# Optimization experiments

Hardware: AMD Instinct MI355X
Metric: run time of the kernel (lower is better)

The kernel has to match this reference:

```python
import jax, jax.numpy as jnp
import numpy as np

EPS = 1e-12
SHRINK = 0.0025

def _l2norm(x, axis=1):
    return x / jnp.maximum(jnp.linalg.norm(x, axis=axis, keepdims=True), EPS)

def setup_inputs() -> dict:
    key = jax.random.key(0)
    ks = jax.random.split(key, 6)
    N, C, H, W = 32, 512, 32, 32
    mem_dim, spatial = 512, H * W
    hid = spatial // 2
    x = jax.random.normal(ks[0], (N, C, H, W), dtype=jnp.float32)
    memory = jax.random.normal(ks[1], (mem_dim, spatial), dtype=jnp.float32)
    memory = _l2norm(memory, axis=1)  # buffer is L2-normalized at init
    w1 = jax.random.normal(ks[2], (hid, spatial), dtype=jnp.float32) * 0.02
    b1 = jax.random.normal(ks[3], (hid,), dtype=jnp.float32) * 0.02
    w2 = jax.random.normal(ks[4], (spatial, hid), dtype=jnp.float32) * 0.02
    b2 = jax.random.normal(ks[5], (spatial,), dtype=jnp.float32) * 0.02
    return {"x": x, "memory": memory, "w1": w1, "b1": b1, "w2": w2, "b2": b2}

def reference(x, memory, w1, b1, w2, b2):
    N, C, H, W = x.shape
    mem_dim = memory.shape[0]
    input_flat = x.reshape(N * C, H * W)
    input_norm = _l2norm(input_flat, axis=1)
    # shared MLP over memory bank: Linear -> ReLU -> Linear -> ReLU
    h = jax.nn.relu(memory @ w1.T + b1)
    mem_proc = jax.nn.relu(h @ w2.T + b2)
    memory_norm = _l2norm(mem_proc, axis=1)
    # addressing: cosine sim -> softmax -> hard shrink -> L1 renorm
    att = jax.nn.softmax(input_norm @ memory_norm.T, axis=1)  # [N*C, M]
    att = jax.nn.relu(att - SHRINK)
    att = att / jnp.maximum(att.sum(axis=1, keepdims=True), EPS)  # p=1 norm (att >= 0)
    output = (att @ memory_norm).reshape(N, C, H, W)
    att_channel_avg = att.reshape(N, C, mem_dim).mean(axis=1)  # [N, M]
    att_spatial = jnp.broadcast_to(att_channel_avg[:, :, None, None], (N, mem_dim, H, W))
    return output, att_spatial, input_flat, memory_norm, att
```

## Files before the change

### kernel.cpp

```cpp
#include <hip/hip_runtime.h>

typedef float  f32x4  __attribute__((ext_vector_type(4)));
typedef __bf16 bf16x8 __attribute__((ext_vector_type(8)));
typedef __bf16 bf16x4 __attribute__((ext_vector_type(4)));

#define L2EPS   1e-12f
#define SHRINKC 0.0025f


__device__ __forceinline__ bf16x8 pack_bf16(f32x4 v0, f32x4 v1) {
  bf16x8 r;
  r[0] = (__bf16)v0[0]; r[1] = (__bf16)v0[1]; r[2] = (__bf16)v0[2]; r[3] = (__bf16)v0[3];
  r[4] = (__bf16)v1[0]; r[5] = (__bf16)v1[1]; r[6] = (__bf16)v1[2]; r[7] = (__bf16)v1[3];
  return r;
}

__device__ __forceinline__ bf16x8 load_cvt_bf16x8(const float* p) {
  const f32x4* q = (const f32x4*)p;
  return pack_bf16(q[0], q[1]);
}

__device__ __forceinline__ float dot4(f32x4 v) {
  return v[0]*v[0] + v[1]*v[1] + v[2]*v[2] + v[3]*v[3];
}

__global__ __launch_bounds__(64) void gemm1(
    const float* __restrict__ A, const float* __restrict__ B,
    const float* __restrict__ bias, float* __restrict__ C,
    float* __restrict__ attsum) {
  const int bid = blockIdx.y * gridDim.x + blockIdx.x;
  attsum[bid * 64 + threadIdx.x] = 0.f;

  const int K = 1024, N = 512;
  const int r0   = blockIdx.x * 32;
  const int n0   = blockIdx.y * 32;
  const int lane = threadIdx.x & 63;
  const int quad = lane >> 4;
  const int m    = lane & 15;

  f32x4 acc[2][2] = {};
  for (int k0 = 0; k0 < K; k0 += 32) {
    const int kk = k0 + quad * 8;
    bf16x8 a[2], b[2];
    #pragma unroll
    for (int rg = 0; rg < 2; ++rg)
      a[rg] = load_cvt_bf16x8(A + (size_t)(r0 + rg * 16 + m) * K + kk);
    #pragma unroll
    for (int cf = 0; cf < 2; ++cf)
      b[cf] = load_cvt_bf16x8(B + (size_t)(n0 + cf * 16 + m) * K + kk);
    #pragma unroll
    for (int rg = 0; rg < 2; ++rg)
      #pragma unroll
      for (int cf = 0; cf < 2; ++cf)
        acc[rg][cf] = __builtin_amdgcn_mfma_f32_16x16x32_bf16(a[rg], b[cf], acc[rg][cf], 0, 0, 0);
  }
  #pragma unroll
  for (int rg = 0; rg < 2; ++rg)
    #pragma unroll
    for (int cf = 0; cf < 2; ++cf) {
      const int n = n0 + cf * 16 + m;
      const float bv = bias[n];
      #pragma unroll
      for (int vi = 0; vi < 4; ++vi) {
        const int r = r0 + rg * 16 + quad * 4 + vi;
        C[(size_t)r * N + n] = fmaxf(acc[rg][cf][vi] + bv, 0.f);
      }
    }
}

__global__ __launch_bounds__(64) void gemm2(
    const float* __restrict__ A, const float* __restrict__ B,
    const float* __restrict__ bias, float* __restrict__ C) {
  const int K = 512, N = 1024;
  const int r0   = blockIdx.x * 32;
  const int n0   = blockIdx.y * 32;
  const int lane = threadIdx.x & 63;
  const int quad = lane >> 4;
  const int m    = lane & 15;

  f32x4 acc[2][2] = {};
  for (int k0 = 0; k0 < K; k0 += 32) {
    const int kk = k0 + quad * 8;
    bf16x8 a[2], b[2];
    #pragma unroll
    for (int rg = 0; rg < 2; ++rg)
      a[rg] = load_cvt_bf16x8(A + (size_t)(r0 + rg * 16 + m) * K + kk);
    #pragma unroll
    for (int cf = 0; cf < 2; ++cf)
      b[cf] = load_cvt_bf16x8(B + (size_t)(n0 + cf * 16 + m) * K + kk);
    #pragma unroll
    for (int rg = 0; rg < 2; ++rg)
      #pragma unroll
      for (int cf = 0; cf < 2; ++cf)
        acc[rg][cf] = __builtin_amdgcn_mfma_f32_16x16x32_bf16(a[rg], b[cf], acc[rg][cf], 0, 0, 0);
  }
  #pragma unroll
  for (int rg = 0; rg < 2; ++rg)
    #pragma unroll
    for (int cf = 0; cf < 2; ++cf) {
      const int n = n0 + cf * 16 + m;
      const float bv = bias[n];
      #pragma unroll
      for (int vi = 0; vi < 4; ++vi) {
        const int r = r0 + rg * 16 + quad * 4 + vi;
        C[(size_t)r * N + n] = fmaxf(acc[rg][cf][vi] + bv, 0.f);
      }
    }
}

__global__ __launch_bounds__(256) void norm_rows(
    const float* __restrict__ mp, float* __restrict__ mn_f32,
    __bf16* __restrict__ mn_bf16) {
  const int r = blockIdx.x;
  const int tid = threadIdx.x;
  const f32x4 v = *(const f32x4*)(mp + (size_t)r * 1024 + tid * 4);
  float ss = dot4(v);
  #pragma unroll
  for (int d = 1; d < 64; d <<= 1) ss += __shfl_xor(ss, d);
  __shared__ float wsum[4];
  __shared__ float invs;
  if ((tid & 63) == 0) wsum[tid >> 6] = ss;
  __syncthreads();
  if (tid == 0) {
    float t = wsum[0] + wsum[1] + wsum[2] + wsum[3];
    invs = 1.f / fmaxf(sqrtf(t), L2EPS);
  }
  __syncthreads();
  const float iv = invs;
  f32x4 o = v * iv;
  *(f32x4*)(mn_f32 + (size_t)r * 1024 + tid * 4) = o;
  bf16x4 ob;
  ob[0] = (__bf16)o[0]; ob[1] = (__bf16)o[1]; ob[2] = (__bf16)o[2]; ob[3] = (__bf16)o[3];
  *(bf16x4*)(mn_bf16 + (size_t)r * 1024 + tid * 4) = ob;
}

__global__ __launch_bounds__(256) void attend(
    const float* __restrict__ x, const __bf16* __restrict__ Mn,
    const float* __restrict__ Mnf, float* __restrict__ out_flat,
    float* __restrict__ out_out, float* __restrict__ out_att,
    float* __restrict__ attsum) {
  __shared__ float red[2][4][32];
  const int r0   = blockIdx.x * 32;
  const int tid  = threadIdx.x;
  const int wave = tid >> 6;
  const int lane = tid & 63;
  const int quad = lane >> 4;
  const int m    = lane & 15;
  const int n0w  = wave * 128;

  float ss0 = 0.f, ss1 = 0.f;
  f32x4 acc[8][2] = {};
  for (int k0 = 0; k0 < 1024; k0 += 32) {
    const int kk = k0 + quad * 8;
    bf16x8 b[2];
    f32x4 v0a, v0b, v1a, v1b;
    {
      const f32x4* q = (const f32x4*)(x + (size_t)(r0 + m) * 1024 + kk);
      v0a = q[0]; v0b = q[1];
      b[0] = pack_bf16(v0a, v0b);
      ss0 += dot4(v0a) + dot4(v0b);
    }
    {
      const f32x4* q = (const f32x4*)(x + (size_t)(r0 + 16 + m) * 1024 + kk);
      v1a = q[0]; v1b = q[1];
      b[1] = pack_bf16(v1a, v1b);
      ss1 += dot4(v1a) + dot4(v1b);
    }
    if (wave == 0) {
      float* d0 = out_flat + (size_t)(r0 + m) * 1024 + kk;
      float* d1 = out_flat + (size_t)(r0 + 16 + m) * 1024 + kk;
      *(f32x4*)d0 = v0a; *(f32x4*)(d0 + 4) = v0b;
      *(f32x4*)d1 = v1a; *(f32x4*)(d1 + 4) = v1b;
    }
    #pragma unroll
    for (int nf = 0; nf < 8; ++nf) {
      const bf16x8 a = *(const bf16x8*)(Mn + (size_t)(n0w + nf * 16 + m) * 1024 + kk);
      acc[nf][0] = __builtin_amdgcn_mfma_f32_16x16x32_bf16(a, b[0], acc[nf][0], 0, 0, 0);
      acc[nf][1] = __builtin_amdgcn_mfma_f32_16x16x32_bf16(a, b[1], acc[nf][1], 0, 0, 0);
    }
  }
  ss0 += __shfl_xor(ss0, 16); ss0 += __shfl_xor(ss0, 32);
  ss1 += __shfl_xor(ss1, 16); ss1 += __shfl_xor(ss1, 32);
  const float iv0 = 1.f / fmaxf(sqrtf(ss0), L2EPS);
  const float iv1 = 1.f / fmaxf(sqrtf(ss1), L2EPS);

  float se0 = 0.f, se1 = 0.f;
  #pragma unroll
  for (int nf = 0; nf < 8; ++nf)
    #pragma unroll
    for (int vi = 0; vi < 4; ++vi) {
      const float e0 = __expf(acc[nf][0][vi] * iv0);
      const float e1 = __expf(acc[nf][1][vi] * iv1);
      acc[nf][0][vi] = e0; acc[nf][1][vi] = e1;
      se0 += e0; se1 += e1;
    }
  se0 += __shfl_xor(se0, 16); se0 += __shfl_xor(se0, 32);
  se1 += __shfl_xor(se1, 16); se1 += __shfl_xor(se1, 32);
  if (quad == 0) { red[0][wave][m] = se0; red[0][wave][16 + m] = se1; }
  __syncthreads();
  const float te0 = red[0][0][m] + red[0][1][m] + red[0][2][m] + red[0][3][m];
  const float te1 = red[0][0][16 + m] + red[0][1][16 + m] + red[0][2][16 + m] + red[0][3][16 + m];
  const float ie0 = 1.f / te0;
  const float ie1 = 1.f / te1;

  float rs0 = 0.f, rs1 = 0.f;
  #pragma unroll
  for (int nf = 0; nf < 8; ++nf)
    #pragma unroll
    for (int vi = 0; vi < 4; ++vi) {
      const float s0 = fmaxf(acc[nf][0][vi] * ie0 - SHRINKC, 0.f);
      const float s1 = fmaxf(acc[nf][1][vi] * ie1 - SHRINKC, 0.f);
      acc[nf][0][vi] = s0; acc[nf][1][vi] = s1;
      rs0 += s0; rs1 += s1;
    }
  rs0 += __shfl_xor(rs0, 16); rs0 += __shfl_xor(rs0, 32);
  rs1 += __shfl_xor(rs1, 16); rs1 += __shfl_xor(rs1, 32);
  if (quad == 0) { red[1][wave][m] = rs0; red[1][wave][16 + m] = rs1; }
  __syncthreads();
  const float tr0 = red[1][0][m] + red[1][1][m] + red[1][2][m] + red[1][3][m];
  const float tr1 = red[1][0][16 + m] + red[1][1][16 + m] + red[1][2][16 + m] + red[1][3][16 + m];
  const float ir0 = 1.f / fmaxf(tr0, L2EPS);
  const float ir1 = 1.f / fmaxf(tr1, L2EPS);

  #pragma unroll
  for (int nf = 0; nf < 8; ++nf) {
    acc[nf][0] *= ir0;
    acc[nf][1] *= ir1;
    *(f32x4*)(out_att + (size_t)(r0 + m)      * 512 + n0w + nf * 16 + quad * 4) = acc[nf][0];
    *(f32x4*)(out_att + (size_t)(r0 + 16 + m) * 512 + n0w + nf * 16 + quad * 4) = acc[nf][1];
  }
  __threadfence_block();
  const int any = __syncthreads_or(tr0 + tr1 > 0.f);

  if (!any) {
    const f32x4 z = {0.f, 0.f, 0.f, 0.f};
    float* dst = out_out + (size_t)r0 * 1024;
    for (int idx = tid; idx < 32 * 1024 / 4; idx += 256)
      *(f32x4*)(dst + idx * 4) = z;
  } else {
    const int nimg = r0 >> 9;
    #pragma unroll
    for (int nf = 0; nf < 8; ++nf) {
      f32x4 v = acc[nf][0] + acc[nf][1];
      #pragma unroll
      for (int d = 1; d < 16; d <<= 1) {
        v[0] += __shfl_xor(v[0], d); v[1] += __shfl_xor(v[1], d);
        v[2] += __shfl_xor(v[2], d); v[3] += __shfl_xor(v[3], d);
      }
      if (m == 0) {
        const int c = n0w + nf * 16 + quad * 4;
        atomicAdd(&attsum[nimg * 512 + c + 0], v[0]);
        atomicAdd(&attsum[nimg * 512 + c + 1], v[1]);
        atomicAdd(&attsum[nimg * 512 + c + 2], v[2]);
        atomicAdd(&attsum[nimg * 512 + c + 3], v[3]);
      }
    }
    const int c0 = tid * 4;
    for (int rr = 0; rr < 32; ++rr) {
      const float* arow = out_att + (size_t)(r0 + rr) * 512;
      f32x4 o = {0.f, 0.f, 0.f, 0.f};
      for (int mm = 0; mm < 512; ++mm) {
        const float a = arow[mm];
        o += a * (*(const f32x4*)(Mnf + (size_t)mm * 1024 + c0));
      }
      *(f32x4*)(out_out + (size_t)(r0 + rr) * 1024 + c0) = o;
    }
  }
}

__global__ __launch_bounds__(256) void spread(
    const float* __restrict__ attsum, float* __restrict__ out_sp) {
  const int base = blockIdx.x * 8;
  #pragma unroll
  for (int p = 0; p < 8; ++p) {
    const int nm = base + p;
    const float v = attsum[nm] * (1.f / 512.f);
    const f32x4 vv = {v, v, v, v};
    *(f32x4*)(out_sp + (size_t)nm * 1024 + threadIdx.x * 4) = vv;
  }
}


extern "C" void kernel_launch(void* const* d_in, const int* in_sizes, int n_in,
                              void* d_out, int out_size, void* d_ws, size_t ws_size,
                              hipStream_t stream) {
  const float* x      = (const float*)d_in[0];
  const float* memory = (const float*)d_in[1];
  const float* w1     = (const float*)d_in[2];
  const float* b1     = (const float*)d_in[3];
  const float* w2     = (const float*)d_in[4];
  const float* b2     = (const float*)d_in[5];

  float* out = (float*)d_out;
  float* out_output = out;
  float* out_attsp  = out + 16777216;
  float* out_flat   = out + 33554432;
  float* out_mnorm  = out + 50331648;
  float* out_att    = out + 50855936;

  char* ws = (char*)d_ws;
  float*  h      = (float*)ws;
  float*  mp     = (float*)(ws + (1 << 20));
  __bf16* mnb    = (__bf16*)(ws + (1 << 20) + (2 << 20));
  float*  attsum = (float*)(ws + (1 << 20) + (2 << 20) + (1 << 20));

  gemm1<<<dim3(16, 16), 64, 0, stream>>>(memory, w1, b1, h, attsum);
  gemm2<<<dim3(16, 32), 64, 0, stream>>>(h, w2, b2, mp);
  norm_rows<<<512, 256, 0, stream>>>(mp, out_mnorm, mnb);
  attend<<<512, 256, 0, stream>>>(x, mnb, out_mnorm, out_flat, out_output, out_att, attsum);
  spread<<<2048, 256, 0, stream>>>(attsum, out_attsp);
}
```

Baseline: 410.8 us.

## Fuse second MLP GEMM with row L2 normalization; use nontemporal stores

Merges gemm2 and norm_rows into one kernel. Each 256-thread block computes full 1024-wide rows, reduces the squared norms through shuffles and shared memory, and writes the normalized fp32 and bf16 outputs directly, which removes one launch and the intermediate buffer. The zero-fill and spread stores become nontemporal. The tradeoff is a grid of only 16 blocks for gemm2n, with 32 accumulators per thread, so parallelism is much lower than the previous 512-block launch.

New measurement: 529.4 us. 28.9% more time.

```diff
diff --git a/kernel.cpp b/kernel.cpp
--- a/kernel.cpp
+++ b/kernel.cpp
@@ -68,70 +68,84 @@
     }
 }
 
-__global__ __launch_bounds__(64) void gemm2(
+__global__ __launch_bounds__(256) void gemm2n(
     const float* __restrict__ A, const float* __restrict__ B,
-    const float* __restrict__ bias, float* __restrict__ C) {
-  const int K = 512, N = 1024;
+    const float* __restrict__ bias, float* __restrict__ mn_f32,
+    __bf16* __restrict__ mn_bf16) {
+  const int K = 512;
   const int r0   = blockIdx.x * 32;
-  const int n0   = blockIdx.y * 32;
-  const int lane = threadIdx.x & 63;
-  const int quad = lane >> 4;
+  const int tid  = threadIdx.x;
+  const int w    = tid >> 6;
+  const int lane = tid & 63;
+  const int q    = lane >> 4;
   const int m    = lane & 15;
-
-  f32x4 acc[2][2] = {};
+  const int n0w  = w * 256;
+
+  f32x4 acc[16][2] = {};
   for (int k0 = 0; k0 < K; k0 += 32) {
-    const int kk = k0 + quad * 8;
-    bf16x8 a[2], b[2];
-    #pragma unroll
-    for (int rg = 0; rg < 2; ++rg)
-      a[rg] = load_cvt_bf16x8(A + (size_t)(r0 + rg * 16 + m) * K + kk);
-    #pragma unroll
-    for (int cf = 0; cf < 2; ++cf)
-      b[cf] = load_cvt_bf16x8(B + (size_t)(n0 + cf * 16 + m) * K + kk);
-    #pragma unroll
-    for (int rg = 0; rg < 2; ++rg)
-      #pragma unroll
-      for (int cf = 0; cf < 2; ++cf)
-        acc[rg][cf] = __builtin_amdgcn_mfma_f32_16x16x32_bf16(a[rg], b[cf], acc[rg][cf], 0, 0, 0);
+    const int kk = k0 + q * 8;
+    bf16x8 a[2];
+    a[0] = load_cvt_bf16x8(A + (size_t)(r0 + m) * K + kk);
+    a[1] = load_cvt_bf16x8(A + (size_t)(r0 + 16 + m) * K + kk);
+    #pragma unroll
+    for (int nf = 0; nf < 16; ++nf) {
+      const bf16x8 b = load_cvt_bf16x8(B + (size_t)(n0w + nf * 16 + m) * K + kk);
+      acc[nf][0] = __builtin_amdgcn_mfma_f32_16x16x32_bf16(a[0], b, acc[nf][0], 0, 0, 0);
+      acc[nf][1] = __builtin_amdgcn_mfma_f32_16x16x32_bf16(a[1], b, acc[nf][1], 0, 0, 0);
+    }
+  }
+  float s[2][4] = {};
+  #pragma unroll
+  for (int nf = 0; nf < 16; ++nf) {
+    const float bv = bias[n0w + nf * 16 + m];
+    #pragma unroll
+    for (int rg = 0; rg < 2; ++rg)
+      #pragma unroll
+      for (int vi = 0; vi < 4; ++vi) {
+        const float v = fmaxf(acc[nf][rg][vi] + bv, 0.f);
+        acc[nf][rg][vi] = v;
+        s[rg][vi] += v * v;
+      }
   }
   #pragma unroll
   for (int rg = 0; rg < 2; ++rg)
     #pragma unroll
-    for (int cf = 0; cf < 2; ++cf) {
-      const int n = n0 + cf * 16 + m;
-      const float bv = bias[n];
+    for (int vi = 0; vi < 4; ++vi) {
+      float t = s[rg][vi];
+      t += __shfl_xor(t, 1); t += __shfl_xor(t, 2);
+      t += __shfl_xor(t, 4); t += __shfl_xor(t, 8);
+      s[rg][vi] = t;
+    }
+  __shared__ float red[4][32];
+  if (m == 0) {
+    #pragma unroll
+    for (int rg = 0; rg < 2; ++rg)
+      #pragma unroll
+      for (int vi = 0; vi < 4; ++vi)
+        red[w][rg * 16 + q * 4 + vi] = s[rg][vi];
+  }
+  __syncthreads();
+  float inv[2][4];
+  #pragma unroll
+  for (int rg = 0; rg < 2; ++rg)
+    #pragma unroll
+    for (int vi = 0; vi < 4; ++vi) {
+      const int row = rg * 16 + q * 4 + vi;
+      const float t = red[0][row] + red[1][row] + red[2][row] + red[3][row];
+      inv[rg][vi] = 1.f / fmaxf(sqrtf(t), L2EPS);
+    }
+  #pragma unroll
+  for (int nf = 0; nf < 16; ++nf)
+    #pragma unroll
+    for (int rg = 0; rg < 2; ++rg)
       #pragma unroll
       for (int vi = 0; vi < 4; ++vi) {
-        const int r = r0 + rg * 16 + quad * 4 + vi;
-        C[(size_t)r * N + n] = fmaxf(acc[rg][cf][vi] + bv, 0.f);
-      }
-    }
-}
-
-__global__ __launch_bounds__(256) void norm_rows(
-    const float* __restrict__ mp, float* __restrict__ mn_f32,
-    __bf16* __restrict__ mn_bf16) {
-  const int r = blockIdx.x;
-  const int tid = threadIdx.x;
-  const f32x4 v = *(const f32x4*)(mp + (size_t)r * 1024 + tid * 4);
-  float ss = dot4(v);
-  #pragma unroll
-  for (int d = 1; d < 64; d <<= 1) ss += __shfl_xor(ss, d);
-  __shared__ float wsum[4];
-  __shared__ float invs;
-  if ((tid & 63) == 0) wsum[tid >> 6] = ss;
-  __syncthreads();
-  if (tid == 0) {
-    float t = wsum[0] + wsum[1] + wsum[2] + wsum[3];
-    invs = 1.f / fmaxf(sqrtf(t), L2EPS);
-  }
-  __syncthreads();
-  const float iv = invs;
-  f32x4 o = v * iv;
-  *(f32x4*)(mn_f32 + (size_t)r * 1024 + tid * 4) = o;
-  bf16x4 ob;
-  ob[0] = (__bf16)o[0]; ob[1] = (__bf16)o[1]; ob[2] = (__bf16)o[2]; ob[3] = (__bf16)o[3];
-  *(bf16x4*)(mn_bf16 + (size_t)r * 1024 + tid * 4) = ob;
+        const int r = r0 + rg * 16 + q * 4 + vi;
+        const int c = n0w + nf * 16 + m;
+        const float v = acc[nf][rg][vi] * inv[rg][vi];
+        mn_f32[(size_t)r * 1024 + c] = v;
+        mn_bf16[(size_t)r * 1024 + c] = (__bf16)v;
+      }
 }
 
 __global__ __launch_bounds__(256) void attend(
@@ -236,7 +250,7 @@
     const f32x4 z = {0.f, 0.f, 0.f, 0.f};
     float* dst = out_out + (size_t)r0 * 1024;
     for (int idx = tid; idx < 32 * 1024 / 4; idx += 256)
-      *(f32x4*)(dst + idx * 4) = z;
+      __builtin_nontemporal_store(z, (f32x4*)(dst + idx * 4));
   } else {
     const int nimg = r0 >> 9;
     #pragma unroll
@@ -276,7 +290,7 @@
     const int nm = base + p;
     const float v = attsum[nm] * (1.f / 512.f);
     const f32x4 vv = {v, v, v, v};
-    *(f32x4*)(out_sp + (size_t)nm * 1024 + threadIdx.x * 4) = vv;
+    __builtin_nontemporal_store(vv, (f32x4*)(out_sp + (size_t)nm * 1024 + threadIdx.x * 4));
   }
 }
 
@@ -300,13 +314,11 @@
 
   char* ws = (char*)d_ws;
   float*  h      = (float*)ws;
-  float*  mp     = (float*)(ws + (1 << 20));
-  __bf16* mnb    = (__bf16*)(ws + (1 << 20) + (2 << 20));
-  float*  attsum = (float*)(ws + (1 << 20) + (2 << 20) + (1 << 20));
+  __bf16* mnb    = (__bf16*)(ws + (1 << 20));
+  float*  attsum = (float*)(ws + (1 << 20) + (1 << 20));
 
   gemm1<<<dim3(16, 16), 64, 0, stream>>>(memory, w1, b1, h, attsum);
-  gemm2<<<dim3(16, 32), 64, 0, stream>>>(h, w2, b2, mp);
-  norm_rows<<<512, 256, 0, stream>>>(mp, out_mnorm, mnb);
+  gemm2n<<<16, 256, 0, stream>>>(h, w2, b2, out_mnorm, mnb);
   attend<<<512, 256, 0, stream>>>(x, mnb, out_mnorm, out_flat, out_output, out_att, attsum);
   spread<<<2048, 256, 0, stream>>>(attsum, out_attsp);
 }
```
